# Performance work log

Measured on AMD Instinct MI355X. Metric: run time of the kernel, lower is better.

Reference implementation:

```python
import jax, jax.numpy as jnp
import numpy as np

ALPHA = 0.4  # matches init alpha
V = 500_000   # variables
F = 2_000_000  # clauses
E = 3 * F      # 3-SAT literal edges
B = 32         # CNF instances in batch


def setup_inputs() -> dict:
    key = jax.random.key(0)
    k1, k2, k3 = jax.random.split(key, 3)
    variable_prediction = jax.random.uniform(k1, (V, 1), dtype=jnp.float32)
    label = jax.random.uniform(k2, (V, 1), dtype=jnp.float32)
    # graph_map[0]: variable index per edge; graph_map[1]: clause index (3 lits/clause, sorted)
    var_idx = jax.random.randint(k3, (E,), 0, V, dtype=jnp.int64)
    fun_idx = jnp.repeat(jnp.arange(F, dtype=jnp.int64), 3)
    graph_map = jnp.stack([var_idx, fun_idx])
    batch_variable_map = (jnp.arange(V, dtype=jnp.int64) * B) // V
    batch_function_map = (jnp.arange(F, dtype=jnp.int64) * B) // F
    # literal polarity +/-1
    sign = jax.random.bernoulli(jax.random.fold_in(key, 7), 0.5, (E, 1))
    edge_feature = jnp.where(sign, 1.0, -1.0).astype(jnp.float32)
    meta_data = jnp.zeros((1,), dtype=jnp.float32)
    global_step = jnp.full((1,), 100.0, dtype=jnp.float32)
    eps = jnp.float32(1e-10)
    max_coeff = jnp.float32(10.0)
    loss_sharpness = 5
    return dict(variable_prediction=variable_prediction, label=label,
                graph_map=graph_map, batch_variable_map=batch_variable_map,
                batch_function_map=batch_function_map, edge_feature=edge_feature,
                meta_data=meta_data, global_step=global_step, eps=eps,
                max_coeff=max_coeff, loss_sharpness=loss_sharpness)


def reference(variable_prediction, label, graph_map, batch_variable_map,
              batch_function_map, edge_feature, meta_data, global_step, eps,
              max_coeff, loss_sharpness):
    # coeff = min(global_step^alpha, max_coeff)
    coeff = jnp.minimum(global_step[0] ** ALPHA, max_coeff)
    var_idx = graph_map[0]
    fun_idx = graph_map[1]
    f_num = batch_function_map.shape[0]
    ef = edge_feature[:, 0]                       # [E], +/-1
    # sparse mm [E,V] (values=edge_feature) @ variable_prediction -> gather*sign
    edge_values = ef * variable_prediction[var_idx, 0] + (1.0 - ef) * 0.5  # [E]
    weights = jnp.exp(coeff * edge_values)        # [E]
    # function_mask mm == segment sum over clauses
    nominator = jax.ops.segment_sum(weights * edge_values, fun_idx,
                                    num_segments=f_num, indices_are_sorted=True)
    denominator = jax.ops.segment_sum(weights, fun_idx,
                                      num_segments=f_num, indices_are_sorted=True)
    clause_value = denominator / jnp.maximum(nominator, eps)
    clause_value = 1.0 + (clause_value - 1.0) ** loss_sharpness
    return jnp.mean(jnp.log(jnp.maximum(clause_value, eps)))
```

## Files before the change

kernel.cpp:

```cpp
#include <hip/hip_runtime.h>

#define TPB 256
#define FPB 256

__global__ __launch_bounds__(TPB) void sat_main_kernel(
    const float* __restrict__ vp,
    const int*   __restrict__ var_idx,
    const float* __restrict__ ef,
    const float* __restrict__ gs,
    const float* __restrict__ epsp,
    const float* __restrict__ maxcp,
    const int*   __restrict__ lsp,
    double*      __restrict__ partial,
    int F, long long E)
{
    __shared__ int   s_idx[FPB * 3];
    __shared__ float s_ef [FPB * 3];

    const int tid = threadIdx.x;
    const long long blk = blockIdx.x;
    const long long ebase = blk * (long long)(FPB * 3);

    #pragma unroll
    for (int i = tid; i < FPB * 3; i += TPB) {
        long long g = ebase + i;
        if (g < E) {
            s_idx[i] = var_idx[g];
            s_ef [i] = ef[g];
        }
    }
    __syncthreads();

    const float coeff = fminf(powf(gs[0], 0.4f), maxcp[0]);
    const float eps   = epsp[0];
    const int   ls    = lsp[0];

    const long long f = blk * (long long)FPB + tid;
    float lg = 0.0f;
    if (f < (long long)F) {
        float nom = 0.0f, den = 0.0f;
        #pragma unroll
        for (int k = 0; k < 3; ++k) {
            const float e = s_ef[tid * 3 + k];
            const float v = vp[s_idx[tid * 3 + k]];
            const float ev = fmaf(e, v, (1.0f - e) * 0.5f);
            const float w  = __expf(coeff * ev);
            nom = fmaf(w, ev, nom);
            den += w;
        }
        const float cv = den / fmaxf(nom, eps);
        const float d  = cv - 1.0f;
        float p = 1.0f;
        for (int i = 0; i < ls; ++i) p *= d;
        const float cvv = 1.0f + p;
        lg = __logf(fmaxf(cvv, eps));
    }

    #pragma unroll
    for (int off = 32; off > 0; off >>= 1)
        lg += __shfl_down(lg, off, 64);

    __shared__ double s_part[TPB / 64];
    if ((tid & 63) == 0) s_part[tid >> 6] = (double)lg;
    __syncthreads();
    if (tid == 0) {
        double s = 0.0;
        #pragma unroll
        for (int w = 0; w < TPB / 64; ++w) s += s_part[w];
        partial[blk] = s;
    }
}

__global__ __launch_bounds__(256) void sat_reduce_kernel(
    const double* __restrict__ partial, int n, float* __restrict__ out, int F)
{
    const int tid = threadIdx.x;
    double s = 0.0;
    for (int i = tid; i < n; i += 256) s += partial[i];

    __shared__ double sm[256];
    sm[tid] = s;
    __syncthreads();
    #pragma unroll
    for (int off = 128; off > 0; off >>= 1) {
        if (tid < off) sm[tid] += sm[tid + off];
        __syncthreads();
    }
    if (tid == 0) out[0] = (float)(sm[0] / (double)F);
}

extern "C" void kernel_launch(void* const* d_in, const int* in_sizes, int n_in,
                              void* d_out, int out_size, void* d_ws, size_t ws_size,
                              hipStream_t stream) {
    const float* vp      = (const float*)d_in[0];
    const int*   gm      = (const int*)  d_in[2];
    const float* ef      = (const float*)d_in[5];
    const float* gs      = (const float*)d_in[7];
    const float* epsp    = (const float*)d_in[8];
    const float* maxcp   = (const float*)d_in[9];
    const int*   lsp     = (const int*)  d_in[10];

    const long long E = (long long)in_sizes[5];
    const int F = in_sizes[4];

    double* partial = (double*)d_ws;
    const int nblocks = (F + FPB - 1) / FPB;

    sat_main_kernel<<<nblocks, TPB, 0, stream>>>(
        vp, gm, ef, gs, epsp, maxcp, lsp, partial, F, E);
    sat_reduce_kernel<<<1, 256, 0, stream>>>(partial, nblocks, (float*)d_out, F);
}
```

Measured before the change: 45.18 us.

## Process four clauses per thread with vectorized nontemporal loads, dropping LDS staging

Each thread now handles four clauses, so it reads 12 contiguous edge indices and signs as three 16-byte vector loads using nontemporal hints. This replaces the shared-memory staging and its barrier. All 12 variable gathers are issued before any computation to raise memory-level parallelism, and the grid shrinks by four times. The trade-offs are more registers per thread, fewer waves to hide the random gathers, and a scalar tail path for the final partial block.

```diff
diff --git a/kernel.cpp b/kernel.cpp
--- a/kernel.cpp
+++ b/kernel.cpp
@@ -1,7 +1,11 @@
 #include <hip/hip_runtime.h>
 
 #define TPB 256
-#define FPB 256
+#define FPT 4
+#define FPB (TPB * FPT)
+
+typedef int   i32x4 __attribute__((ext_vector_type(4)));
+typedef float f32x4 __attribute__((ext_vector_type(4)));
 
 __global__ __launch_bounds__(TPB) void sat_main_kernel(
     const float* __restrict__ vp,
@@ -12,48 +16,79 @@
     const float* __restrict__ maxcp,
     const int*   __restrict__ lsp,
     double*      __restrict__ partial,
-    int F, long long E)
+    int F)
 {
-    __shared__ int   s_idx[FPB * 3];
-    __shared__ float s_ef [FPB * 3];
-
     const int tid = threadIdx.x;
-    const long long blk = blockIdx.x;
-    const long long ebase = blk * (long long)(FPB * 3);
-
-    #pragma unroll
-    for (int i = tid; i < FPB * 3; i += TPB) {
-        long long g = ebase + i;
-        if (g < E) {
-            s_idx[i] = var_idx[g];
-            s_ef [i] = ef[g];
-        }
-    }
-    __syncthreads();
-
     const float coeff = fminf(powf(gs[0], 0.4f), maxcp[0]);
     const float eps   = epsp[0];
     const int   ls    = lsp[0];
 
-    const long long f = blk * (long long)FPB + tid;
+    const long long fbase = (long long)blockIdx.x * FPB + (long long)tid * FPT;
     float lg = 0.0f;
-    if (f < (long long)F) {
-        float nom = 0.0f, den = 0.0f;
+
+    if (fbase + FPT <= (long long)F) {
+        const long long eb = fbase * 3;
+
+        const i32x4* ip = (const i32x4*)(var_idx + eb);
+        i32x4 ia = __builtin_nontemporal_load(ip);
+        i32x4 ib = __builtin_nontemporal_load(ip + 1);
+        i32x4 ic = __builtin_nontemporal_load(ip + 2);
+
+        const f32x4* epv = (const f32x4*)(ef + eb);
+        f32x4 ea  = __builtin_nontemporal_load(epv);
+        f32x4 eb4 = __builtin_nontemporal_load(epv + 1);
+        f32x4 ec  = __builtin_nontemporal_load(epv + 2);
+
+        int idx[12] = { ia.x, ia.y, ia.z, ia.w,
+                        ib.x, ib.y, ib.z, ib.w,
+                        ic.x, ic.y, ic.z, ic.w };
+        float e[12] = { ea.x, ea.y, ea.z, ea.w,
+                        eb4.x, eb4.y, eb4.z, eb4.w,
+                        ec.x, ec.y, ec.z, ec.w };
+
+        float v[12];
         #pragma unroll
-        for (int k = 0; k < 3; ++k) {
-            const float e = s_ef[tid * 3 + k];
-            const float v = vp[s_idx[tid * 3 + k]];
-            const float ev = fmaf(e, v, (1.0f - e) * 0.5f);
-            const float w  = __expf(coeff * ev);
-            nom = fmaf(w, ev, nom);
-            den += w;
+        for (int k = 0; k < 12; ++k) v[k] = vp[idx[k]];
+
+        #pragma unroll
+        for (int q = 0; q < FPT; ++q) {
+            float nom = 0.0f, den = 0.0f;
+            #pragma unroll
+            for (int j = 0; j < 3; ++j) {
+                const float e1 = e[q * 3 + j];
+                const float ev = fmaf(e1, v[q * 3 + j], (1.0f - e1) * 0.5f);
+                const float w  = __expf(coeff * ev);
+                nom = fmaf(w, ev, nom);
+                den += w;
+            }
+            const float cv = den / fmaxf(nom, eps);
+            const float d  = cv - 1.0f;
+            float p = 1.0f;
+            for (int i = 0; i < ls; ++i) p *= d;
+            lg += __logf(fmaxf(1.0f + p, eps));
         }
-        const float cv = den / fmaxf(nom, eps);
-        const float d  = cv - 1.0f;
-        float p = 1.0f;
-        for (int i = 0; i < ls; ++i) p *= d;
-        const float cvv = 1.0f + p;
-        lg = __logf(fmaxf(cvv, eps));
+    } else {
+        for (int q = 0; q < FPT; ++q) {
+            const long long f = fbase + q;
+            if (f < (long long)F) {
+                const long long eb = f * 3;
+                float nom = 0.0f, den = 0.0f;
+                #pragma unroll
+                for (int j = 0; j < 3; ++j) {
+                    const float e1 = ef[eb + j];
+                    const float vv = vp[var_idx[eb + j]];
+                    const float ev = fmaf(e1, vv, (1.0f - e1) * 0.5f);
+                    const float w  = __expf(coeff * ev);
+                    nom = fmaf(w, ev, nom);
+                    den += w;
+                }
+                const float cv = den / fmaxf(nom, eps);
+                const float d  = cv - 1.0f;
+                float p = 1.0f;
+                for (int i = 0; i < ls; ++i) p *= d;
+                lg += __logf(fmaxf(1.0f + p, eps));
+            }
+        }
     }
 
     #pragma unroll
@@ -67,7 +102,7 @@
         double s = 0.0;
         #pragma unroll
         for (int w = 0; w < TPB / 64; ++w) s += s_part[w];
-        partial[blk] = s;
+        partial[blockIdx.x] = s;
     }
 }
 
@@ -100,13 +135,12 @@
     const float* maxcp   = (const float*)d_in[9];
     const int*   lsp     = (const int*)  d_in[10];
 
-    const long long E = (long long)in_sizes[5];
     const int F = in_sizes[4];
 
     double* partial = (double*)d_ws;
     const int nblocks = (F + FPB - 1) / FPB;
 
     sat_main_kernel<<<nblocks, TPB, 0, stream>>>(
-        vp, gm, ef, gs, epsp, maxcp, lsp, partial, F, E);
+        vp, gm, ef, gs, epsp, maxcp, lsp, partial, F);
     sat_reduce_kernel<<<1, 256, 0, stream>>>(partial, nblocks, (float*)d_out, F);
 }
```

Measured after the change: 42.62 us. -5.7%, faster.
